# Kernel tuning notes

Hardware: AMD Instinct MI355X
Metric: run time of the kernel (lower is better)

## Reference

```python
import jax, jax.numpy as jnp
import numpy as np

# Graph block sizes (outermost -> innermost), fixed fanout neighbor sampling
N0, N1, N2, N3 = 256000, 25600, 2560, 512
D_IN, D_H, D_OUT = 1024, 256, 19
FANOUTS = (10, 10, 5)


def _lin(key, d_in, d_out):
    return jax.random.normal(key, (d_in, d_out), jnp.float32) / np.sqrt(d_in)


def setup_inputs() -> dict:
    key = jax.random.key(0)
    ks = jax.random.split(key, 13)
    x = jax.random.normal(ks[0], (N0, D_IN), jnp.float32)
    # DGL block convention: dst nodes are the first n_dst src nodes, so
    # h_dst = h[:n_dst]. Neighbor tables index into the src node set.
    nbr0 = jax.random.randint(ks[1], (N1, FANOUTS[0]), 0, N0)
    nbr1 = jax.random.randint(ks[2], (N2, FANOUTS[1]), 0, N1)
    nbr2 = jax.random.randint(ks[3], (N3, FANOUTS[2]), 0, N2)
    return {
        "x": x, "nbr0": nbr0, "nbr1": nbr1, "nbr2": nbr2,
        "Wself0": _lin(ks[4], D_IN, D_H), "Wneigh0": _lin(ks[5], D_IN, D_H),
        "b0": jnp.zeros((D_H,), jnp.float32),
        "Wself1": _lin(ks[6], D_H, D_H), "Wneigh1": _lin(ks[7], D_H, D_H),
        "b1": jnp.zeros((D_H,), jnp.float32),
        "Wself2": _lin(ks[8], D_H, D_OUT), "Wneigh2": _lin(ks[9], D_H, D_OUT),
        "b2": jnp.zeros((D_OUT,), jnp.float32),
    }


def sage_layer(h, nbr, Wself, Wneigh, b):
    # SAGEConv('mean'): fc_self(h_dst) + fc_neigh(mean over sampled neighbors)
    n_dst = nbr.shape[0]
    h_neigh = jnp.mean(h[nbr], axis=1)  # [n_dst, fanout, d] -> [n_dst, d]
    return h[:n_dst] @ Wself + h_neigh @ Wneigh + b


def reference(x, nbr0, nbr1, nbr2,
              Wself0, Wneigh0, b0,
              Wself1, Wneigh1, b1,
              Wself2, Wneigh2, b2):
    # Dropout is identity in eval mode; activation = relu.
    h = jax.nn.relu(sage_layer(x, nbr0, Wself0, Wneigh0, b0))
    h = jax.nn.relu(sage_layer(h, nbr1, Wself1, Wneigh1, b1))
    return sage_layer(h, nbr2, Wself2, Wneigh2, b2)  # [N3, n_classes]
```

## Files before the change

### kernel.cpp

```cpp
#include <hip/hip_runtime.h>
#include <hip/hip_bf16.h>


typedef __attribute__((ext_vector_type(4))) float f32x4;
typedef __attribute__((ext_vector_type(8))) short s16x8;

__device__ __forceinline__ unsigned short f2bf_u16(float f) {
  unsigned int u = __float_as_uint(f);
  u += 0x7fffu + ((u >> 16) & 1u);
  return (unsigned short)(u >> 16);
}

__device__ __forceinline__ void gload16(const void* g, void* l) {
  __builtin_amdgcn_global_load_lds(
      (const __attribute__((address_space(1))) unsigned int*)g,
      (__attribute__((address_space(3))) unsigned int*)l, 16, 0, 0);
}

__global__ void prep_wcat2(const float* __restrict__ Ws0, const float* __restrict__ Wn0,
                           unsigned short* __restrict__ Wt0,
                           const float* __restrict__ Ws1, const float* __restrict__ Wn1,
                           unsigned short* __restrict__ Wt1) {
  int idx = blockIdx.x * 256 + threadIdx.x;
  if (idx < 256 * 2048) {
    int n = idx >> 11, k = idx & 2047;
    float v = (k < 1024) ? Ws0[k * 256 + n] : Wn0[(k - 1024) * 256 + n];
    Wt0[idx] = f2bf_u16(v);
  } else {
    int i2 = idx - 256 * 2048;
    if (i2 < 256 * 512) {
      int n = i2 >> 9, k = i2 & 511;
      float v = (k < 256) ? Ws1[k * 256 + n] : Wn1[(k - 256) * 256 + n];
      Wt1[i2] = f2bf_u16(v);
    }
  }
}

template <int D, int F>
__global__ void gather_cat(const float* __restrict__ h,
                           const int* __restrict__ nbr,
                           unsigned short* __restrict__ out) {
  const int i = blockIdx.x;
  const int c = threadIdx.x;
  int idx[F];
#pragma unroll
  for (int f = 0; f < F; ++f) idx[f] = nbr[(size_t)i * F + f];
  constexpr float inv = 1.0f / (float)F;

  float4 s = reinterpret_cast<const float4*>(h + (size_t)i * D)[c];
  ushort4 us = {f2bf_u16(s.x), f2bf_u16(s.y), f2bf_u16(s.z), f2bf_u16(s.w)};
  reinterpret_cast<ushort4*>(out + (size_t)i * 2 * D)[c] = us;

  float ax = 0.f, ay = 0.f, az = 0.f, aw = 0.f;
#pragma unroll
  for (int f = 0; f < F; ++f) {
    float4 v = reinterpret_cast<const float4*>(h + (size_t)idx[f] * D)[c];
    ax += v.x; ay += v.y; az += v.z; aw += v.w;
  }
  ushort4 un = {f2bf_u16(ax * inv), f2bf_u16(ay * inv), f2bf_u16(az * inv), f2bf_u16(aw * inv)};
  reinterpret_cast<ushort4*>(out + (size_t)i * 2 * D + D)[c] = un;
}

template <bool RELU>
__global__ __launch_bounds__(256) void gemm_gl(
    const unsigned short* __restrict__ A,
    const unsigned short* __restrict__ Bt,
    const float* __restrict__ bias,
    float* __restrict__ C,
    int Kc) {
  constexpr int BM = 64, BN = 256, BK = 64;
  __shared__ __align__(16) unsigned short As[BM * BK];
  __shared__ __align__(16) unsigned short Bs[BN * BK];

  const int tid = threadIdx.x;
  const int wid = tid >> 6, lane = tid & 63;
  const size_t bm = (size_t)blockIdx.x * BM;

  const int srow = (wid << 3) + (lane >> 3);
  const int gs = (lane & 7) ^ ((lane >> 3) & 7);
  const unsigned short* gA = A + (bm + srow) * (size_t)Kc + gs * 8;
  const unsigned short* gB = Bt + (size_t)srow * Kc + gs * 8;
  unsigned short* lA = As + wid * 512;
  unsigned short* lB = Bs + wid * 512;

  f32x4 acc[4][4];
#pragma unroll
  for (int mi = 0; mi < 4; ++mi)
#pragma unroll
    for (int ni = 0; ni < 4; ++ni)
      acc[mi][ni] = (f32x4){0.f, 0.f, 0.f, 0.f};

  const int l15 = lane & 15, lq = lane >> 4, l7 = lane & 7;

  for (int kt = 0; kt < Kc; kt += BK) {
    gload16(gA + kt, lA);
    gload16(gA + 32 * (size_t)Kc + kt, lA + 2048);
#pragma unroll
    for (int p = 0; p < 8; ++p)
      gload16(gB + p * 32 * (size_t)Kc + kt, lB + p * 2048);
    __syncthreads();

#pragma unroll
    for (int ks = 0; ks < 2; ++ks) {
      const int gr = ((ks << 2) + lq) ^ l7;
      s16x8 af[4], bf_[4];
#pragma unroll
      for (int mi = 0; mi < 4; ++mi) {
        const int row = mi * 16 + l15;
        af[mi] = *reinterpret_cast<const s16x8*>(
            reinterpret_cast<const char*>(As) + row * 128 + gr * 16);
      }
#pragma unroll
      for (int ni = 0; ni < 4; ++ni) {
        const int row = wid * 64 + ni * 16 + l15;
        bf_[ni] = *reinterpret_cast<const s16x8*>(
            reinterpret_cast<const char*>(Bs) + row * 128 + gr * 16);
      }
#pragma unroll
      for (int mi = 0; mi < 4; ++mi)
#pragma unroll
        for (int ni = 0; ni < 4; ++ni)
          acc[mi][ni] = __builtin_amdgcn_mfma_f32_16x16x32_bf16(af[mi], bf_[ni], acc[mi][ni], 0, 0, 0);
    }
    __syncthreads();
  }

#pragma unroll
  for (int mi = 0; mi < 4; ++mi) {
    const size_t r0 = bm + mi * 16 + lq * 4;
#pragma unroll
    for (int ni = 0; ni < 4; ++ni) {
      const int c = wid * 64 + ni * 16 + l15;
      const float bv = bias[c];
#pragma unroll
      for (int rr = 0; rr < 4; ++rr) {
        float v = acc[mi][ni][rr] + bv;
        if (RELU) v = fmaxf(v, 0.f);
        C[(r0 + rr) * (size_t)BN + c] = v;
      }
    }
  }
}

__global__ void out_fused(const float* __restrict__ h1, const int* __restrict__ nbr,
                          const float* __restrict__ Ws, const float* __restrict__ Wn,
                          const float* __restrict__ b, float* __restrict__ out) {
  const int i = blockIdx.x, t = threadIdx.x;
  __shared__ float row[512];
  __shared__ float part[8][32];
  row[t] = h1[(size_t)i * 256 + t];
  float s = 0.f;
#pragma unroll
  for (int f = 0; f < 5; ++f) s += h1[(size_t)nbr[i * 5 + f] * 256 + t];
  row[256 + t] = s * 0.2f;
  __syncthreads();
  const int n = t & 31, seg = t >> 5;
  float p = 0.f;
  if (n < 19) {
#pragma unroll
    for (int e = 0; e < 64; ++e) {
      const int k = seg * 64 + e;
      const float w = (k < 256) ? Ws[k * 19 + n] : Wn[(k - 256) * 19 + n];
      p += row[k] * w;
    }
  }
  part[seg][n] = p;
  __syncthreads();
  if (t < 19) {
    float sm = b[t];
#pragma unroll
    for (int g = 0; g < 8; ++g) sm += part[g][t];
    out[(size_t)i * 19 + t] = sm;
  }
}

extern "C" void kernel_launch(void* const* d_in, const int* in_sizes, int n_in,
                              void* d_out, int out_size, void* d_ws, size_t ws_size,
                              hipStream_t stream) {
  const float* x    = (const float*)d_in[0];
  const int*   nbr0 = (const int*)d_in[1];
  const int*   nbr1 = (const int*)d_in[2];
  const int*   nbr2 = (const int*)d_in[3];
  const float* Ws0  = (const float*)d_in[4];
  const float* Wn0  = (const float*)d_in[5];
  const float* b0   = (const float*)d_in[6];
  const float* Ws1  = (const float*)d_in[7];
  const float* Wn1  = (const float*)d_in[8];
  const float* b1   = (const float*)d_in[9];
  const float* Ws2  = (const float*)d_in[10];
  const float* Wn2  = (const float*)d_in[11];
  const float* b2   = (const float*)d_in[12];
  float* out = (float*)d_out;

  char* ws = (char*)d_ws;
  unsigned short* A0   = (unsigned short*)(ws);
  unsigned short* Wt0  = (unsigned short*)(ws + 104857600);
  float*          h0   = (float*)(ws + 105906176);
  unsigned short* cat1 = (unsigned short*)(ws + 132120576);
  unsigned short* Wt1  = (unsigned short*)(ws + 134742016);
  float*          h1   = (float*)(ws + 135004160);

  prep_wcat2<<<(256 * 2048 + 256 * 512 + 255) / 256, 256, 0, stream>>>(
      Ws0, Wn0, Wt0, Ws1, Wn1, Wt1);

  gather_cat<1024, 10><<<25600, 256, 0, stream>>>(x, nbr0, A0);
  gemm_gl<true><<<400, 256, 0, stream>>>(A0, Wt0, b0, h0, 2048);

  gather_cat<256, 10><<<2560, 64, 0, stream>>>(h0, nbr1, cat1);
  gemm_gl<true><<<40, 256, 0, stream>>>(cat1, Wt1, b1, h1, 512);

  out_fused<<<512, 256, 0, stream>>>(h1, nbr2, Ws2, Wn2, b2, out);
}
```

Before: 307.4 us.

## Fuse weight prep into layer-0 gather; widen per-thread loads and use nontemporal stores

Merges the weight transpose/convert kernel into the layer-0 gather kernel as 40 extra blocks, removing one launch and letting the weight conversion overlap the gather. Each gather thread now handles 8 floats (two float4 loads) with 128-thread blocks and writes a 16-byte bf16 pack with nontemporal stores, so the A0 output does not pollute cache. The trade-off is fewer threads in flight per row and a tail of prep blocks that loop over the weights serially.

```diff
diff --git a/kernel.cpp b/kernel.cpp
--- a/kernel.cpp
+++ b/kernel.cpp
@@ -11,27 +11,67 @@
   return (unsigned short)(u >> 16);
 }
 
+__device__ __forceinline__ s16x8 pack_bf16x8(const float4& a, const float4& b) {
+  s16x8 w;
+  w[0] = (short)f2bf_u16(a.x); w[1] = (short)f2bf_u16(a.y);
+  w[2] = (short)f2bf_u16(a.z); w[3] = (short)f2bf_u16(a.w);
+  w[4] = (short)f2bf_u16(b.x); w[5] = (short)f2bf_u16(b.y);
+  w[6] = (short)f2bf_u16(b.z); w[7] = (short)f2bf_u16(b.w);
+  return w;
+}
+
 __device__ __forceinline__ void gload16(const void* g, void* l) {
   __builtin_amdgcn_global_load_lds(
       (const __attribute__((address_space(1))) unsigned int*)g,
       (__attribute__((address_space(3))) unsigned int*)l, 16, 0, 0);
 }
 
-__global__ void prep_wcat2(const float* __restrict__ Ws0, const float* __restrict__ Wn0,
-                           unsigned short* __restrict__ Wt0,
-                           const float* __restrict__ Ws1, const float* __restrict__ Wn1,
-                           unsigned short* __restrict__ Wt1) {
-  int idx = blockIdx.x * 256 + threadIdx.x;
-  if (idx < 256 * 2048) {
-    int n = idx >> 11, k = idx & 2047;
-    float v = (k < 1024) ? Ws0[k * 256 + n] : Wn0[(k - 1024) * 256 + n];
-    Wt0[idx] = f2bf_u16(v);
+__global__ __launch_bounds__(128) void gather0_prep(
+    const float* __restrict__ x, const int* __restrict__ nbr,
+    unsigned short* __restrict__ A0,
+    const float* __restrict__ Ws0, const float* __restrict__ Wn0,
+    unsigned short* __restrict__ Wt0,
+    const float* __restrict__ Ws1, const float* __restrict__ Wn1,
+    unsigned short* __restrict__ Wt1) {
+  constexpr int NDST = 25600, D = 1024, F = 10;
+  const int bid = blockIdx.x, t = threadIdx.x;
+
+  if (bid < NDST) {
+    const size_t i = bid;
+    int idx[F];
+#pragma unroll
+    for (int f = 0; f < F; ++f) idx[f] = nbr[i * F + f];
+
+    const float4* ps = reinterpret_cast<const float4*>(x + i * D) + 2 * t;
+    float4 s0 = ps[0], s1 = ps[1];
+    __builtin_nontemporal_store(
+        pack_bf16x8(s0, s1), reinterpret_cast<s16x8*>(A0 + i * 2 * D) + t);
+
+    float4 a0 = make_float4(0.f, 0.f, 0.f, 0.f);
+    float4 a1 = make_float4(0.f, 0.f, 0.f, 0.f);
+#pragma unroll
+    for (int f = 0; f < F; ++f) {
+      const float4* p = reinterpret_cast<const float4*>(x + (size_t)idx[f] * D) + 2 * t;
+      float4 u0 = p[0], u1 = p[1];
+      a0.x += u0.x; a0.y += u0.y; a0.z += u0.z; a0.w += u0.w;
+      a1.x += u1.x; a1.y += u1.y; a1.z += u1.z; a1.w += u1.w;
+    }
+    constexpr float inv = 1.0f / (float)F;
+    a0.x *= inv; a0.y *= inv; a0.z *= inv; a0.w *= inv;
+    a1.x *= inv; a1.y *= inv; a1.z *= inv; a1.w *= inv;
+    __builtin_nontemporal_store(
+        pack_bf16x8(a0, a1), reinterpret_cast<s16x8*>(A0 + i * 2 * D + D) + t);
   } else {
-    int i2 = idx - 256 * 2048;
-    if (i2 < 256 * 512) {
-      int n = i2 >> 9, k = i2 & 511;
+    const int pt = (bid - NDST) * 128 + t;
+    for (int e = pt; e < 256 * 2048; e += 5120) {
+      int n = e >> 11, k = e & 2047;
+      float v = (k < 1024) ? Ws0[k * 256 + n] : Wn0[(k - 1024) * 256 + n];
+      Wt0[e] = f2bf_u16(v);
+    }
+    for (int e = pt; e < 256 * 512; e += 5120) {
+      int n = e >> 9, k = e & 511;
       float v = (k < 256) ? Ws1[k * 256 + n] : Wn1[(k - 256) * 256 + n];
-      Wt1[i2] = f2bf_u16(v);
+      Wt1[e] = f2bf_u16(v);
     }
   }
 }
@@ -200,10 +240,7 @@
   unsigned short* Wt1  = (unsigned short*)(ws + 134742016);
   float*          h1   = (float*)(ws + 135004160);
 
-  prep_wcat2<<<(256 * 2048 + 256 * 512 + 255) / 256, 256, 0, stream>>>(
-      Ws0, Wn0, Wt0, Ws1, Wn1, Wt1);
-
-  gather_cat<1024, 10><<<25600, 256, 0, stream>>>(x, nbr0, A0);
+  gather0_prep<<<25600 + 40, 128, 0, stream>>>(x, nbr0, A0, Ws0, Wn0, Wt0, Ws1, Wn1, Wt1);
   gemm_gl<true><<<400, 256, 0, stream>>>(A0, Wt0, b0, h0, 2048);
 
   gather_cat<256, 10><<<2560, 64, 0, stream>>>(h0, nbr1, cat1);
```

Result: faster. 292.1 us (-5.0%).

## Project unique neighbor rows before averaging in first SAGE layer

Applied to the files above, without the earlier changes.

Layer 0 now applies Wneigh to the rows of x that are actually referenced, then gathers and averages the projected 256-wide rows. Before, the kernel gathered ten 1024-wide fp32 rows per destination and concatenated them into a bf16 buffer. A flag/scan/compact pipeline builds the list of unique source nodes and a position map. The neighbor GEMM loads fp32 x directly and converts it to bf16 in registers, and the self GEMM fuses the bias, the averaged neighbor term and the ReLU. The aim is to cut the dominant gather traffic on x and the intermediate A0 buffer. In exchange it adds several small launches, a larger GEMM over about 160k rows, and bf16 rounding of the projected values before averaging.

```diff
diff --git a/kernel.cpp b/kernel.cpp
--- a/kernel.cpp
+++ b/kernel.cpp
@@ -10,35 +10,235 @@
   u += 0x7fffu + ((u >> 16) & 1u);
   return (unsigned short)(u >> 16);
 }
-
+__device__ __forceinline__ float bf2f(unsigned short u) {
+  return __uint_as_float(((unsigned int)u) << 16);
+}
+__device__ __forceinline__ s16x8 pack_bf16x8(const float4& a, const float4& b) {
+  s16x8 w;
+  w[0] = (short)f2bf_u16(a.x); w[1] = (short)f2bf_u16(a.y);
+  w[2] = (short)f2bf_u16(a.z); w[3] = (short)f2bf_u16(a.w);
+  w[4] = (short)f2bf_u16(b.x); w[5] = (short)f2bf_u16(b.y);
+  w[6] = (short)f2bf_u16(b.z); w[7] = (short)f2bf_u16(b.w);
+  return w;
+}
+__device__ __forceinline__ s16x8 pack_bf16x8v(f32x4 a, f32x4 b) {
+  s16x8 w;
+  w[0] = (short)f2bf_u16(a[0]); w[1] = (short)f2bf_u16(a[1]);
+  w[2] = (short)f2bf_u16(a[2]); w[3] = (short)f2bf_u16(a[3]);
+  w[4] = (short)f2bf_u16(b[0]); w[5] = (short)f2bf_u16(b[1]);
+  w[6] = (short)f2bf_u16(b[2]); w[7] = (short)f2bf_u16(b[3]);
+  return w;
+}
 __device__ __forceinline__ void gload16(const void* g, void* l) {
   __builtin_amdgcn_global_load_lds(
       (const __attribute__((address_space(1))) unsigned int*)g,
       (__attribute__((address_space(3))) unsigned int*)l, 16, 0, 0);
 }
 
-__global__ void prep_wcat2(const float* __restrict__ Ws0, const float* __restrict__ Wn0,
-                           unsigned short* __restrict__ Wt0,
-                           const float* __restrict__ Ws1, const float* __restrict__ Wn1,
-                           unsigned short* __restrict__ Wt1) {
+__global__ __launch_bounds__(256) void zero_flags(unsigned int* flags_u32) {
+  int i = blockIdx.x * 256 + threadIdx.x;
+  if (i < 64000) flags_u32[i] = 0;
+}
+
+__global__ __launch_bounds__(256) void set_flags(const int* __restrict__ nbr0,
+                                                 unsigned char* __restrict__ flags) {
+  int i = blockIdx.x * 256 + threadIdx.x;
+  flags[nbr0[i]] = 1;
+}
+
+__global__ __launch_bounds__(256) void count_flags(const unsigned char* __restrict__ flags,
+                                                   int* __restrict__ bsum) {
+  const int b = blockIdx.x, t = threadIdx.x;
+  int v = (int)flags[b * 256 + t];
+  for (int o = 32; o > 0; o >>= 1) v += __shfl_down(v, o);
+  __shared__ int s[4];
+  if ((t & 63) == 0) s[t >> 6] = v;
+  __syncthreads();
+  if (t == 0) bsum[b] = s[0] + s[1] + s[2] + s[3];
+}
+
+__global__ __launch_bounds__(1024) void scan_sums(const int* __restrict__ bsum,
+                                                  int* __restrict__ offs,
+                                                  int* __restrict__ cnt) {
+  __shared__ int s[1024];
+  const int t = threadIdx.x;
+  const int mine = (t < 1000) ? bsum[t] : 0;
+  s[t] = mine;
+  __syncthreads();
+  for (int o = 1; o < 1024; o <<= 1) {
+    int v = (t >= o) ? s[t - o] : 0;
+    __syncthreads();
+    s[t] += v;
+    __syncthreads();
+  }
+  if (t < 1000) offs[t] = s[t] - mine;
+  if (t == 999) *cnt = s[999];
+}
+
+__global__ __launch_bounds__(256) void scatter_flags(const unsigned char* __restrict__ flags,
+                                                     const int* __restrict__ offs,
+                                                     int* __restrict__ list,
+                                                     int* __restrict__ pos) {
+  const int b = blockIdx.x, t = threadIdx.x, n = b * 256 + t;
+  const int f = (int)flags[n];
+  __shared__ int s[256];
+  s[t] = f;
+  __syncthreads();
+  for (int o = 1; o < 256; o <<= 1) {
+    int v = (t >= o) ? s[t - o] : 0;
+    __syncthreads();
+    s[t] += v;
+    __syncthreads();
+  }
+  if (f) {
+    const int p = offs[b] + s[t] - 1;
+    list[p] = n;
+    pos[n] = p;
+  }
+}
+
+__global__ __launch_bounds__(256) void prep3(
+    const float* __restrict__ Ws0, const float* __restrict__ Wn0,
+    const float* __restrict__ Ws1, const float* __restrict__ Wn1,
+    unsigned short* __restrict__ Wts0, unsigned short* __restrict__ Wtn0,
+    unsigned short* __restrict__ Wt1) {
   int idx = blockIdx.x * 256 + threadIdx.x;
-  if (idx < 256 * 2048) {
-    int n = idx >> 11, k = idx & 2047;
-    float v = (k < 1024) ? Ws0[k * 256 + n] : Wn0[(k - 1024) * 256 + n];
-    Wt0[idx] = f2bf_u16(v);
+  if (idx < 262144) {
+    int n = idx >> 10, k = idx & 1023;
+    Wts0[idx] = f2bf_u16(Ws0[k * 256 + n]);
+  } else if (idx < 524288) {
+    int e = idx - 262144, n = e >> 10, k = e & 1023;
+    Wtn0[e] = f2bf_u16(Wn0[k * 256 + n]);
   } else {
-    int i2 = idx - 256 * 2048;
-    if (i2 < 256 * 512) {
-      int n = i2 >> 9, k = i2 & 511;
-      float v = (k < 256) ? Ws1[k * 256 + n] : Wn1[(k - 256) * 256 + n];
-      Wt1[i2] = f2bf_u16(v);
-    }
-  }
+    int e = idx - 524288;
+    if (e < 131072) {
+      int n = e >> 9, k = e & 511;
+      Wt1[e] = f2bf_u16(k < 256 ? Ws1[k * 256 + n] : Wn1[(k - 256) * 256 + n]);
+    }
+  }
+}
+
+template <bool INDIRECT>
+__global__ __launch_bounds__(256) void sage_gemm_f32a(
+    const float* __restrict__ X, const int* __restrict__ list,
+    const int* __restrict__ cnt_p, const unsigned short* __restrict__ Bt,
+    const float* __restrict__ hn, const float* __restrict__ bias,
+    unsigned short* __restrict__ Zout, float* __restrict__ Cout) {
+  constexpr int BK = 64, Kc = 1024;
+  __shared__ __align__(16) unsigned short As[64 * 64];
+  __shared__ __align__(16) unsigned short Bs[256 * 64];
+  const int tid = threadIdx.x, wid = tid >> 6, lane = tid & 63;
+  const size_t bm = (size_t)blockIdx.x * 64;
+  int cnt = 0;
+  if (INDIRECT) {
+    cnt = *cnt_p;
+    if ((int)bm >= cnt) return;
+  }
+
+  const int arow = tid >> 2, afc = (tid & 3) * 16;
+  size_t asrc;
+  if (INDIRECT) {
+    const int li = (int)bm + arow;
+    asrc = (size_t)((li < cnt) ? list[li] : list[0]);
+  } else {
+    asrc = bm + arow;
+  }
+  const float* gA = X + asrc * Kc + afc;
+  const int g0 = ((tid & 3) * 2) ^ (arow & 7);
+  unsigned short* wA = As + arow * 64;
+
+  const int srow = (wid << 3) + (lane >> 3);
+  const int gs = (lane & 7) ^ ((lane >> 3) & 7);
+  const unsigned short* gB = Bt + (size_t)srow * Kc + gs * 8;
+  unsigned short* lB = Bs + wid * 512;
+
+  f32x4 acc[4][4];
+#pragma unroll
+  for (int mi = 0; mi < 4; ++mi)
+#pragma unroll
+    for (int ni = 0; ni < 4; ++ni) acc[mi][ni] = (f32x4){0.f, 0.f, 0.f, 0.f};
+
+  const int l15 = lane & 15, lq = lane >> 4, l7 = lane & 7;
+
+  const f32x4* p0 = reinterpret_cast<const f32x4*>(gA);
+  f32x4 a0 = __builtin_nontemporal_load(p0 + 0);
+  f32x4 a1 = __builtin_nontemporal_load(p0 + 1);
+  f32x4 a2 = __builtin_nontemporal_load(p0 + 2);
+  f32x4 a3 = __builtin_nontemporal_load(p0 + 3);
+
+  for (int kt = 0; kt < Kc; kt += BK) {
+#pragma unroll
+    for (int p = 0; p < 8; ++p) gload16(gB + p * 32 * (size_t)Kc + kt, lB + p * 2048);
+    *reinterpret_cast<s16x8*>(wA + g0 * 8) = pack_bf16x8v(a0, a1);
+    *reinterpret_cast<s16x8*>(wA + (g0 ^ 1) * 8) = pack_bf16x8v(a2, a3);
+    __syncthreads();
+    if (kt + BK < Kc) {
+      const f32x4* pn = reinterpret_cast<const f32x4*>(gA + kt + BK);
+      a0 = __builtin_nontemporal_load(pn + 0);
+      a1 = __builtin_nontemporal_load(pn + 1);
+      a2 = __builtin_nontemporal_load(pn + 2);
+      a3 = __builtin_nontemporal_load(pn + 3);
+    }
+#pragma unroll
+    for (int ks = 0; ks < 2; ++ks) {
+      const int gr = ((ks << 2) + lq) ^ l7;
+      s16x8 af[4], bf_[4];
+#pragma unroll
+      for (int mi = 0; mi < 4; ++mi)
+        af[mi] = *reinterpret_cast<const s16x8*>(
+            reinterpret_cast<const char*>(As) + (mi * 16 + l15) * 128 + gr * 16);
+#pragma unroll
+      for (int ni = 0; ni < 4; ++ni)
+        bf_[ni] = *reinterpret_cast<const s16x8*>(
+            reinterpret_cast<const char*>(Bs) + (wid * 64 + ni * 16 + l15) * 128 + gr * 16);
+#pragma unroll
+      for (int mi = 0; mi < 4; ++mi)
+#pragma unroll
+        for (int ni = 0; ni < 4; ++ni)
+          acc[mi][ni] = __builtin_amdgcn_mfma_f32_16x16x32_bf16(af[mi], bf_[ni], acc[mi][ni], 0, 0, 0);
+    }
+    __syncthreads();
+  }
+
+#pragma unroll
+  for (int mi = 0; mi < 4; ++mi) {
+    const size_t r0 = bm + mi * 16 + lq * 4;
+#pragma unroll
+    for (int ni = 0; ni < 4; ++ni) {
+      const int c = wid * 64 + ni * 16 + l15;
+      if (INDIRECT) {
+#pragma unroll
+        for (int rr = 0; rr < 4; ++rr)
+          Zout[(r0 + rr) * 256 + c] = f2bf_u16(acc[mi][ni][rr]);
+      } else {
+        const float bv = bias[c];
+#pragma unroll
+        for (int rr = 0; rr < 4; ++rr) {
+          float v = acc[mi][ni][rr] + hn[(r0 + rr) * 256 + c] + bv;
+          Cout[(r0 + rr) * 256 + c] = fmaxf(v, 0.f);
+        }
+      }
+    }
+  }
+}
+
+__global__ __launch_bounds__(64) void gather_mean_z(
+    const unsigned short* __restrict__ z, const int* __restrict__ nbr,
+    const int* __restrict__ pos, float* __restrict__ hn) {
+  const int i = blockIdx.x, t = threadIdx.x;
+  float4 a = make_float4(0.f, 0.f, 0.f, 0.f);
+#pragma unroll
+  for (int f = 0; f < 10; ++f) {
+    const int p = pos[nbr[i * 10 + f]];
+    ushort4 u = *reinterpret_cast<const ushort4*>(z + (size_t)p * 256 + t * 4);
+    a.x += bf2f(u.x); a.y += bf2f(u.y); a.z += bf2f(u.z); a.w += bf2f(u.w);
+  }
+  a.x *= 0.1f; a.y *= 0.1f; a.z *= 0.1f; a.w *= 0.1f;
+  *reinterpret_cast<float4*>(hn + (size_t)i * 256 + t * 4) = a;
 }
 
 template <int D, int F>
-__global__ void gather_cat(const float* __restrict__ h,
-                           const int* __restrict__ nbr,
+__global__ void gather_cat(const float* __restrict__ h, const int* __restrict__ nbr,
                            unsigned short* __restrict__ out) {
   const int i = blockIdx.x;
   const int c = threadIdx.x;
@@ -46,11 +246,9 @@
 #pragma unroll
   for (int f = 0; f < F; ++f) idx[f] = nbr[(size_t)i * F + f];
   constexpr float inv = 1.0f / (float)F;
-
   float4 s = reinterpret_cast<const float4*>(h + (size_t)i * D)[c];
   ushort4 us = {f2bf_u16(s.x), f2bf_u16(s.y), f2bf_u16(s.z), f2bf_u16(s.w)};
   reinterpret_cast<ushort4*>(out + (size_t)i * 2 * D)[c] = us;
-
   float ax = 0.f, ay = 0.f, az = 0.f, aw = 0.f;
 #pragma unroll
   for (int f = 0; f < F; ++f) {
@@ -63,59 +261,42 @@
 
 template <bool RELU>
 __global__ __launch_bounds__(256) void gemm_gl(
-    const unsigned short* __restrict__ A,
-    const unsigned short* __restrict__ Bt,
-    const float* __restrict__ bias,
-    float* __restrict__ C,
-    int Kc) {
-  constexpr int BM = 64, BN = 256, BK = 64;
-  __shared__ __align__(16) unsigned short As[BM * BK];
-  __shared__ __align__(16) unsigned short Bs[BN * BK];
-
-  const int tid = threadIdx.x;
-  const int wid = tid >> 6, lane = tid & 63;
-  const size_t bm = (size_t)blockIdx.x * BM;
-
+    const unsigned short* __restrict__ A, const unsigned short* __restrict__ Bt,
+    const float* __restrict__ bias, float* __restrict__ C, int Kc) {
+  __shared__ __align__(16) unsigned short As[64 * 64];
+  __shared__ __align__(16) unsigned short Bs[256 * 64];
+  const int tid = threadIdx.x, wid = tid >> 6, lane = tid & 63;
+  const size_t bm = (size_t)blockIdx.x * 64;
   const int srow = (wid << 3) + (lane >> 3);
   const int gs = (lane & 7) ^ ((lane >> 3) & 7);
   const unsigned short* gA = A + (bm + srow) * (size_t)Kc + gs * 8;
   const unsigned short* gB = Bt + (size_t)srow * Kc + gs * 8;
   unsigned short* lA = As + wid * 512;
   unsigned short* lB = Bs + wid * 512;
-
   f32x4 acc[4][4];
 #pragma unroll
   for (int mi = 0; mi < 4; ++mi)
 #pragma unroll
-    for (int ni = 0; ni < 4; ++ni)
-      acc[mi][ni] = (f32x4){0.f, 0.f, 0.f, 0.f};
-
+    for (int ni = 0; ni < 4; ++ni) acc[mi][ni] = (f32x4){0.f, 0.f, 0.f, 0.f};
   const int l15 = lane & 15, lq = lane >> 4, l7 = lane & 7;
-
-  for (int kt = 0; kt < Kc; kt += BK) {
+  for (int kt = 0; kt < Kc; kt += 64) {
     gload16(gA + kt, lA);
     gload16(gA + 32 * (size_t)Kc + kt, lA + 2048);
 #pragma unroll
-    for (int p = 0; p < 8; ++p)
-      gload16(gB + p * 32 * (size_t)Kc + kt, lB + p * 2048);
-    __syncthreads();
-
+    for (int p = 0; p < 8; ++p) gload16(gB + p * 32 * (size_t)Kc + kt, lB + p * 2048);
+    __syncthreads();
 #pragma unroll
     for (int ks = 0; ks < 2; ++ks) {
       const int gr = ((ks << 2) + lq) ^ l7;
       s16x8 af[4], bf_[4];
 #pragma unroll
-      for (int mi = 0; mi < 4; ++mi) {
-        const int row = mi * 16 + l15;
+      for (int mi = 0; mi < 4; ++mi)
         af[mi] = *reinterpret_cast<const s16x8*>(
-            reinterpret_cast<const char*>(As) + row * 128 + gr * 16);
-      }
-#pragma unroll
-      for (int ni = 0; ni < 4; ++ni) {
-        const int row = wid * 64 + ni * 16 + l15;
+            reinterpret_cast<const char*>(As) + (mi * 16 + l15) * 128 + gr * 16);
+#pragma unroll
+      for (int ni = 0; ni < 4; ++ni)
         bf_[ni] = *reinterpret_cast<const s16x8*>(
-            reinterpret_cast<const char*>(Bs) + row * 128 + gr * 16);
-      }
+            reinterpret_cast<const char*>(Bs) + (wid * 64 + ni * 16 + l15) * 128 + gr * 16);
 #pragma unroll
       for (int mi = 0; mi < 4; ++mi)
 #pragma unroll
@@ -124,7 +305,6 @@
     }
     __syncthreads();
   }
-
 #pragma unroll
   for (int mi = 0; mi < 4; ++mi) {
     const size_t r0 = bm + mi * 16 + lq * 4;
@@ -136,7 +316,7 @@
       for (int rr = 0; rr < 4; ++rr) {
         float v = acc[mi][ni][rr] + bv;
         if (RELU) v = fmaxf(v, 0.f);
-        C[(r0 + rr) * (size_t)BN + c] = v;
+        C[(r0 + rr) * 256 + c] = v;
       }
     }
   }
@@ -193,21 +373,35 @@
   float* out = (float*)d_out;
 
   char* ws = (char*)d_ws;
-  unsigned short* A0   = (unsigned short*)(ws);
-  unsigned short* Wt0  = (unsigned short*)(ws + 104857600);
-  float*          h0   = (float*)(ws + 105906176);
-  unsigned short* cat1 = (unsigned short*)(ws + 132120576);
-  unsigned short* Wt1  = (unsigned short*)(ws + 134742016);
-  float*          h1   = (float*)(ws + 135004160);
-
-  prep_wcat2<<<(256 * 2048 + 256 * 512 + 255) / 256, 256, 0, stream>>>(
-      Ws0, Wn0, Wt0, Ws1, Wn1, Wt1);
-
-  gather_cat<1024, 10><<<25600, 256, 0, stream>>>(x, nbr0, A0);
-  gemm_gl<true><<<400, 256, 0, stream>>>(A0, Wt0, b0, h0, 2048);
+  unsigned char* flags = (unsigned char*)(ws);
+  int*  bsum = (int*)(ws + 262144);
+  int*  offs = (int*)(ws + 266240);
+  int*  cnt  = (int*)(ws + 270336);
+  int*  list = (int*)(ws + 270592);
+  int*  pos  = (int*)(ws + 1294592);
+  unsigned short* z    = (unsigned short*)(ws + 2318592);
+  float*          hn   = (float*)(ws + 133390592);
+  float*          h0   = (float*)(ws + 159604992);
+  unsigned short* Wts0 = (unsigned short*)(ws + 185819392);
+  unsigned short* Wtn0 = (unsigned short*)(ws + 186343680);
+  unsigned short* Wt1  = (unsigned short*)(ws + 186867968);
+  unsigned short* cat1 = (unsigned short*)(ws + 187130112);
+  float*          h1   = (float*)(ws + 189751552);
+
+  prep3<<<2560, 256, 0, stream>>>(Ws0, Wn0, Ws1, Wn1, Wts0, Wtn0, Wt1);
+  zero_flags<<<250, 256, 0, stream>>>((unsigned int*)flags);
+  set_flags<<<1000, 256, 0, stream>>>(nbr0, flags);
+  count_flags<<<1000, 256, 0, stream>>>(flags, bsum);
+  scan_sums<<<1, 1024, 0, stream>>>(bsum, offs, cnt);
+  scatter_flags<<<1000, 256, 0, stream>>>(flags, offs, list, pos);
+
+  sage_gemm_f32a<true><<<4000, 256, 0, stream>>>(x, list, cnt, Wtn0,
+                                                 nullptr, nullptr, z, nullptr);
+  gather_mean_z<<<25600, 64, 0, stream>>>(z, nbr0, pos, hn);
+  sage_gemm_f32a<false><<<400, 256, 0, stream>>>(x, nullptr, nullptr, Wts0,
+                                                 hn, b0, nullptr, h0);
 
   gather_cat<256, 10><<<2560, 64, 0, stream>>>(h0, nbr1, cat1);
   gemm_gl<true><<<40, 256, 0, stream>>>(cat1, Wt1, b1, h1, 512);
-
   out_fused<<<512, 256, 0, stream>>>(h1, nbr2, Ws2, Wn2, b2, out);
 }
```

Result: slower. 385.3 us (+25.3%).
